# Kernel tuning notes

Hardware: AMD Instinct MI355X
Metric: run time of the kernel (lower is better)

The kernel has to match this reference:

```python
import jax, jax.numpy as jnp
import numpy as np

B, T, E, H, HD = 4, 1500, 1280, 20, 64
SCALING = HD ** -0.5


def setup_inputs() -> dict:
    key = jax.random.key(0)
    ks = jax.random.split(key, 8)
    s = 0.02
    return {
        "hidden_states": jax.random.normal(ks[0], (B, 1, T, E), jnp.float32),
        "attention_mask": jnp.zeros((B, 1, T, T), jnp.float32),
        "Wq": jax.random.normal(ks[1], (H, HD, E), jnp.float32) * s,
        "bq": jax.random.normal(ks[2], (H, HD), jnp.float32) * s,
        "Wk": jax.random.normal(ks[3], (H, HD, E), jnp.float32) * s,
        "Wv": jax.random.normal(ks[4], (H, HD, E), jnp.float32) * s,
        "bv": jax.random.normal(ks[5], (H, HD), jnp.float32) * s,
        "Wo": jax.random.normal(ks[6], (E, E), jnp.float32) * s,
        "bo": jax.random.normal(ks[7], (E,), jnp.float32) * s,
    }


def reference(hidden_states, attention_mask, Wq, bq, Wk, Wv, bv, Wo, bo):
    # hidden_states: [B, 1, T, E] (NHWC with H=1, as in the torch module)
    b, _, t, e = hidden_states.shape
    x = hidden_states[:, 0]  # [B, T, E]
    # Per-head 1x1 Conv2d projections == batched linear over stacked head weights.
    # Scaling is folded into q (the module bakes it into q_proj weights/bias).
    q = (jnp.einsum("bte,hde->bhtd", x, Wq) + bq[None, :, None, :]) * SCALING
    k = jnp.einsum("bse,hde->bhsd", x, Wk)
    v = jnp.einsum("bse,hde->bhsd", x, Wv) + bv[None, :, None, :]
    # attention_mask broadcasts over the head dim (module adds it per head as [B,1,T,S])
    scores = jnp.einsum("bhtd,bhsd->bhts", q, k) + attention_mask  # [B,H,T,S]
    attn = jax.nn.softmax(scores, axis=-1)
    out = jnp.einsum("bhts,bhsd->bhtd", attn, v)  # [B,H,T,HD]
    out = out.transpose(0, 2, 1, 3).reshape(b, t, e)  # concat heads on channel dim
    final = jnp.einsum("bte,fe->btf", out, Wo) + bo  # 1x1 Conv2d out_proj
    return final[:, None, :, :]  # [B,1,T,E]
```

## Files before the change

kernel.cpp:

```cpp
#include <hip/hip_runtime.h>

#define T_LEN 1500
#define TP    1536
#define EDIM  1280
#define NH    20
#define HD    64
#define KDIM  1280

#define LOG2E 1.4426950408889634f

#define OFF_X    ((size_t)0)
#define OFF_AO   ((size_t)0)
#define OFF_W    ((size_t)7700480)
#define OFF_WO   ((size_t)12615680)
#define OFF_Q    ((size_t)14254080)
#define OFF_K    ((size_t)22118400)
#define OFF_VT   ((size_t)29982720)

typedef float  f32x4  __attribute__((ext_vector_type(4)));
typedef float  f32x16 __attribute__((ext_vector_type(16)));
typedef short  s16x8  __attribute__((ext_vector_type(8)));
typedef __bf16 bf16x8 __attribute__((ext_vector_type(8)));
typedef unsigned short u16;
typedef unsigned int   u32;
typedef unsigned int u32x4 __attribute__((ext_vector_type(4)));

__device__ __forceinline__ f32x4 mfma_bf16(s16x8 a, s16x8 b, f32x4 c) {
  return __builtin_amdgcn_mfma_f32_16x16x32_bf16(
      __builtin_bit_cast(bf16x8, a), __builtin_bit_cast(bf16x8, b), c, 0, 0, 0);
}

__device__ __forceinline__ f32x16 mfma32(s16x8 a, s16x8 b, f32x16 c) {
  return __builtin_amdgcn_mfma_f32_32x32x16_bf16(
      __builtin_bit_cast(bf16x8, a), __builtin_bit_cast(bf16x8, b), c, 0, 0, 0);
}

__device__ __forceinline__ u16 f2bf(float f) {
  union { float f; unsigned int u; } a; a.f = f;
  return (u16)((a.u + 0x7fffu + ((a.u >> 16) & 1u)) >> 16);
}

__device__ __forceinline__ float fexp2(float x) {
  return __builtin_amdgcn_exp2f(x);
}

__device__ __forceinline__ void gl_lds16(const u16* g, u16* l) {
  __builtin_amdgcn_global_load_lds(
      (const __attribute__((address_space(1))) unsigned int*)(const void*)g,
      (__attribute__((address_space(3))) unsigned int*)(void*)l, 16, 0, 0);
}


__global__ __launch_bounds__(256) void prep_kernel(
    const float* __restrict__ x, const float* __restrict__ wq,
    const float* __restrict__ wk, const float* __restrict__ wv,
    const float* __restrict__ wo, const float* __restrict__ mask,
    u16* __restrict__ ws, u32* __restrict__ nzflags) {
  const int S0 = 1925120;
  const int S1 = 1228800;
  const int S2 = 409600;
  const int P1 = 46080;
  const int S3 = 2250000;
  const int TOT = S0 + S1 + S2 + 3 * P1 + S3;
  for (int v = blockIdx.x * 256 + threadIdx.x; v < TOT; v += gridDim.x * 256) {
    if (v < S0) {
      int i = v * 4;
      int m = i / EDIM;
      ushort4 o;
      if (m < 6000) {
        float4 f = *(const float4*)(x + i);
        o = make_ushort4(f2bf(f.x), f2bf(f.y), f2bf(f.z), f2bf(f.w));
      } else {
        o = make_ushort4(0, 0, 0, 0);
      }
      *(ushort4*)(ws + OFF_X + i) = o;
    } else if (v < S0 + S1) {
      int j = (v - S0) * 4;
      int n = j / EDIM, e = j - n * EDIM;
      const float* s = (n < 1280) ? wq + (size_t)n * EDIM + e
                     : (n < 2560) ? wk + (size_t)(n - 1280) * EDIM + e
                                  : wv + (size_t)(n - 2560) * EDIM + e;
      float4 f = *(const float4*)s;
      *(ushort4*)(ws + OFF_W + j) = make_ushort4(f2bf(f.x), f2bf(f.y), f2bf(f.z), f2bf(f.w));
    } else if (v < S0 + S1 + S2) {
      int j = (v - S0 - S1) * 4;
      float4 f = *(const float4*)(wo + j);
      *(ushort4*)(ws + OFF_WO + j) = make_ushort4(f2bf(f.x), f2bf(f.y), f2bf(f.z), f2bf(f.w));
    } else if (v < S0 + S1 + S2 + 3 * P1) {
      int p = v - (S0 + S1 + S2);
      ushort4 z = make_ushort4(0, 0, 0, 0);
      if (p < P1) {
        int p4 = p * 4; int bh = p4 / 2304; int rem = p4 - bh * 2304;
        int tt = rem >> 6, d = rem & 63;
        *(ushort4*)(ws + OFF_Q + ((size_t)(bh * TP + 1500 + tt)) * HD + d) = z;
      } else if (p < 2 * P1) {
        int p4 = (p - P1) * 4; int bh = p4 / 2304; int rem = p4 - bh * 2304;
        int tt = rem >> 6, d = rem & 63;
        *(ushort4*)(ws + OFF_K + ((size_t)(bh * TP + 1500 + tt)) * HD + d) = z;
      } else {
        int p4 = (p - 2 * P1) * 4; int bh = p4 / 2304; int rem = p4 - bh * 2304;
        int d = rem / 36, ss = rem - d * 36;
        int t = 1500 + ss;
        int tphys = (t & ~63) | (((((t >> 3) & 7) ^ (d & 7))) << 3) | (t & 7);
        *(ushort4*)(ws + OFF_VT + ((size_t)(bh * HD + d)) * TP + tphys) = z;
      }
    } else {
      int p = v - (S0 + S1 + S2 + 3 * P1);
      int i4 = p * 4;
      int bb = i4 / 2250000;
      int rem = i4 - bb * 2250000;
      int q = rem / 1500;
      int s = rem - q * 1500;
      float4 f = *(const float4*)(mask + (size_t)bb * 2250000 + rem);
      if (f.x != 0.f || f.y != 0.f || f.z != 0.f || f.w != 0.f)
        atomicOr(&nzflags[(bb * 12 + (q >> 7)) * 24 + (s >> 6)], 1u);
    }
  }
}

__device__ __forceinline__ void gemm_mainloop(
    const u16* __restrict__ A, const u16* __restrict__ B,
    int mt, int nt, u16* As, u16* Bs, f32x4 acc[4][4]) {
  const int tid = threadIdx.x;
  const int w = tid >> 6, lane = tid & 63, lg = lane >> 4, lr = lane & 15;
  const int wr = w >> 1, wc = w & 1;
  const int c0 = tid, c1 = tid + 256;
  const u16* a0 = A + (size_t)(mt * 128 + (c0 >> 2)) * KDIM + (c0 & 3) * 8;
  const u16* a1 = A + (size_t)(mt * 128 + (c1 >> 2)) * KDIM + (c1 & 3) * 8;
  const u16* b0 = B + (size_t)(nt * 128 + (c0 >> 2)) * KDIM + (c0 & 3) * 8;
  const u16* b1 = B + (size_t)(nt * 128 + (c1 >> 2)) * KDIM + (c1 & 3) * 8;
  u16* lA0 = As + c0 * 8; u16* lA1 = As + c1 * 8;
  u16* lB0 = Bs + c0 * 8; u16* lB1 = Bs + c1 * 8;
  for (int kt = 0; kt < KDIM / 32; ++kt) {
    gl_lds16(a0 + kt * 32, lA0);
    gl_lds16(a1 + kt * 32, lA1);
    gl_lds16(b0 + kt * 32, lB0);
    gl_lds16(b1 + kt * 32, lB1);
    __syncthreads();
    s16x8 af[4], bg[4];
    #pragma unroll
    for (int i = 0; i < 4; ++i) {
      af[i] = *(const s16x8*)(As + ((wr * 64 + i * 16 + lr) * 32 + lg * 8));
      bg[i] = *(const s16x8*)(Bs + ((wc * 64 + i * 16 + lr) * 32 + lg * 8));
    }
    #pragma unroll
    for (int i = 0; i < 4; ++i)
      #pragma unroll
      for (int j = 0; j < 4; ++j)
        acc[i][j] = mfma_bf16(af[i], bg[j], acc[i][j]);
    __syncthreads();
  }
}

__global__ __launch_bounds__(256) void gemm_qkv_kernel(
    const u16* __restrict__ X, const u16* __restrict__ W,
    const float* __restrict__ bq, const float* __restrict__ bv,
    u16* __restrict__ Qw, u16* __restrict__ Kw, u16* __restrict__ Vtw) {
  __shared__ __align__(16) u16 As[128 * 32];
  __shared__ __align__(16) u16 Bs[128 * 32];
  const int nt = blockIdx.x, mt = blockIdx.y;
  f32x4 acc[4][4] = {};
  gemm_mainloop(X, W, mt, nt, As, Bs, acc);
  const int tid = threadIdx.x;
  const int w = tid >> 6, lane = tid & 63, lg = lane >> 4, lr = lane & 15;
  const int wr = w >> 1, wc = w & 1;
  #pragma unroll
  for (int i = 0; i < 4; ++i) {
    #pragma unroll
    for (int r = 0; r < 4; ++r) {
      int mm = mt * 128 + wr * 64 + i * 16 + lg * 4 + r;
      if (mm >= 6000) continue;
      int bt = mm / 1500, tt = mm - bt * 1500;
      #pragma unroll
      for (int j = 0; j < 4; ++j) {
        int n = nt * 128 + wc * 64 + j * 16 + lr;
        float v = acc[i][j][r];
        if (n < 1280) {
          int hh = n >> 6, d = n & 63;
          Qw[((size_t)(bt * NH + hh) * TP + tt) * HD + d] =
              f2bf((v + bq[n]) * (0.125f * LOG2E));
        } else if (n < 2560) {
          int nn = n - 1280, hh = nn >> 6, d = nn & 63;
          int dp = ((((d >> 3) ^ (tt & 7))) << 3) | (d & 7);
          Kw[((size_t)(bt * NH + hh) * TP + tt) * HD + dp] = f2bf(v);
        } else {
          int nn = n - 2560, hh = nn >> 6, d = nn & 63;
          int tphys = (tt & ~63) | (((((tt >> 3) & 7) ^ (d & 7))) << 3) | (tt & 7);
          Vtw[((size_t)(bt * NH + hh) * HD + d) * TP + tphys] = f2bf(v + bv[nn]);
        }
      }
    }
  }
}

__global__ __launch_bounds__(256) void attn_kernel(
    const u16* __restrict__ Qw, const u16* __restrict__ Kw,
    const u16* __restrict__ Vtw, const float* __restrict__ mask,
    const u32* __restrict__ nzflags, u16* __restrict__ AO) {
  __shared__ __align__(16) u16 Kb[2][64 * 64];
  __shared__ __align__(16) u16 Vb[2][64 * 64];
  const int bhid = blockIdx.y;
  const int bb = bhid / NH, hh = bhid % NH;
  const int tid = threadIdx.x;
  const int w = tid >> 6;
  const int lane = tid & 63;
  const int lq = lane & 31;
  const int hi = lane >> 5;
  const int q0 = blockIdx.x * 128 + w * 32;
  const int qrow = q0 + lq;
  const int qm = qrow < (T_LEN - 1) ? qrow : (T_LEN - 1);
  const u16* Qp = Qw + (size_t)bhid * TP * HD;
  const u16* Kp = Kw + (size_t)bhid * TP * HD;
  const u16* Vp = Vtw + (size_t)bhid * HD * TP;
  const float* mp = mask + (size_t)bb * T_LEN * T_LEN + (size_t)qm * T_LEN;
  const u32* nzp = nzflags + (bb * 12 + blockIdx.x) * 24;

  s16x8 qf[4];
  #pragma unroll
  for (int c = 0; c < 4; ++c)
    qf[c] = *(const s16x8*)(Qp + (size_t)qrow * HD + c * 16 + hi * 8);

  f32x16 O0 = {}, O1 = {};
  float m = -3e38f, l = 0.f;

  {
    gl_lds16(Kp + tid * 8,                 Kb[0] + tid * 8);
    gl_lds16(Kp + 2048 + tid * 8,          Kb[0] + 2048 + tid * 8);
    int r = tid >> 3, g = tid & 7;
    gl_lds16(Vp + (size_t)r * TP + g * 8,          Vb[0] + tid * 8);
    gl_lds16(Vp + (size_t)(r + 32) * TP + g * 8,   Vb[0] + 2048 + tid * 8);
  }
  __syncthreads();

  int buf = 0;
  #pragma unroll 1
  for (int st = 0; st < 24; ++st) {
    const int s0 = st * 64;
    if (st < 23) {
      const int sn = s0 + 64;
      gl_lds16(Kp + (size_t)sn * HD + tid * 8,        Kb[buf ^ 1] + tid * 8);
      gl_lds16(Kp + (size_t)sn * HD + 2048 + tid * 8, Kb[buf ^ 1] + 2048 + tid * 8);
      int r = tid >> 3, g = tid & 7;
      gl_lds16(Vp + (size_t)r * TP + sn + g * 8,        Vb[buf ^ 1] + tid * 8);
      gl_lds16(Vp + (size_t)(r + 32) * TP + sn + g * 8, Vb[buf ^ 1] + 2048 + tid * 8);
    }
    const bool has_mask = nzp[st] != 0u;
    const u16* kb = Kb[buf];
    f32x16 S0a = {}, S1a = {};
    #pragma unroll
    for (int c = 0; c < 4; ++c) {
      int gc = 2 * c + hi;
      int gs = (gc ^ (lq & 7)) << 3;
      s16x8 k0 = *(const s16x8*)(kb + lq * 64 + gs);
      s16x8 k1 = *(const s16x8*)(kb + (32 + lq) * 64 + gs);
      S0a = mfma32(k0, qf[c], S0a);
      S1a = mfma32(k1, qf[c], S1a);
    }
    float p[32];
    #pragma unroll
    for (int r = 0; r < 16; ++r) { p[r] = S0a[r]; p[16 + r] = S1a[r]; }
    if (has_mask) {
      f32x4 mk[2][4];
      #pragma unroll
      for (int sh = 0; sh < 2; ++sh)
        #pragma unroll
        for (int g = 0; g < 4; ++g) {
          int sb = s0 + sh * 32 + 8 * g + 4 * hi;
          if (sb > T_LEN - 4) sb = T_LEN - 4;
          mk[sh][g] = *(const f32x4*)(mp + sb);
        }
      #pragma unroll
      for (int r = 0; r < 16; ++r) {
        p[r]      = fmaf(mk[0][r >> 2][r & 3], LOG2E, p[r]);
        p[16 + r] = fmaf(mk[1][r >> 2][r & 3], LOG2E, p[16 + r]);
      }
    }
    if (st == 23) {
      if (hi) { p[12] = p[13] = p[14] = p[15] = -1e30f; }
      #pragma unroll
      for (int r = 16; r < 32; ++r) p[r] = -1e30f;
    }
    float t1[16];
    #pragma unroll
    for (int r = 0; r < 16; ++r) t1[r] = fmaxf(p[r], p[r + 16]);
    #pragma unroll
    for (int r = 0; r < 8; ++r) t1[r] = fmaxf(t1[r], t1[r + 8]);
    float mx = fmaxf(fmaxf(fmaxf(t1[0], t1[1]), fmaxf(t1[2], t1[3])),
                     fmaxf(fmaxf(t1[4], t1[5]), fmaxf(t1[6], t1[7])));
    mx = fmaxf(mx, __shfl_xor(mx, 32));
    if (!__all(mx <= m + 8.f)) {
      float mn = fmaxf(m, mx);
      float sc = fexp2(m - mn);
      O0 *= sc; O1 *= sc; l *= sc;
      m = mn;
    }
    #pragma unroll
    for (int r = 0; r < 32; ++r) p[r] = fexp2(p[r] - m);
    float s1[16];
    #pragma unroll
    for (int r = 0; r < 16; ++r) s1[r] = p[r] + p[r + 16];
    #pragma unroll
    for (int r = 0; r < 8; ++r) s1[r] += s1[r + 8];
    #pragma unroll
    for (int r = 0; r < 4; ++r) s1[r] += s1[r + 4];
    float rs = (s1[0] + s1[1]) + (s1[2] + s1[3]);
    rs += __shfl_xor(rs, 32);
    l += rs;
    const u16* vb = Vb[buf];
    #pragma unroll
    for (int sh = 0; sh < 2; ++sh) {
      u32 pk[8];
      #pragma unroll
      for (int j = 0; j < 8; ++j)
        asm("v_cvt_pk_bf16_f32 %0, %1, %2"
            : "=v"(pk[j]) : "v"(p[sh * 16 + 2 * j]), "v"(p[sh * 16 + 2 * j + 1]));
      asm("v_permlane32_swap_b32 %0, %1" : "+v"(pk[0]), "+v"(pk[2]));
      asm("v_permlane32_swap_b32 %0, %1" : "+v"(pk[1]), "+v"(pk[3]));
      asm("v_permlane32_swap_b32 %0, %1" : "+v"(pk[4]), "+v"(pk[6]));
      asm("v_permlane32_swap_b32 %0, %1" : "+v"(pk[5]), "+v"(pk[7]));
      u32x4 ta = {pk[0], pk[1], pk[2], pk[3]};
      u32x4 tb = {pk[4], pk[5], pk[6], pk[7]};
      s16x8 pfa = __builtin_bit_cast(s16x8, ta);
      s16x8 pfb = __builtin_bit_cast(s16x8, tb);
      int ga = sh * 4 + hi, gb = sh * 4 + 2 + hi;
      {
        int d = lq;
        s16x8 va = *(const s16x8*)(vb + d * 64 + ((ga ^ (d & 7)) << 3));
        s16x8 vc = *(const s16x8*)(vb + d * 64 + ((gb ^ (d & 7)) << 3));
        O0 = mfma32(va, pfa, O0);
        O0 = mfma32(vc, pfb, O0);
      }
      {
        int d = 32 + lq;
        s16x8 va = *(const s16x8*)(vb + d * 64 + ((ga ^ (d & 7)) << 3));
        s16x8 vc = *(const s16x8*)(vb + d * 64 + ((gb ^ (d & 7)) << 3));
        O1 = mfma32(va, pfa, O1);
        O1 = mfma32(vc, pfb, O1);
      }
    }
    __syncthreads();
    buf ^= 1;
  }

  if (qrow < T_LEN) {
    float inv = 1.f / l;
    size_t base = ((size_t)(bb * T_LEN + qrow)) * EDIM + hh * HD;
    #pragma unroll
    for (int g = 0; g < 4; ++g) {
      ushort4 o0, o1;
      o0.x = f2bf(O0[4 * g + 0] * inv); o0.y = f2bf(O0[4 * g + 1] * inv);
      o0.z = f2bf(O0[4 * g + 2] * inv); o0.w = f2bf(O0[4 * g + 3] * inv);
      o1.x = f2bf(O1[4 * g + 0] * inv); o1.y = f2bf(O1[4 * g + 1] * inv);
      o1.z = f2bf(O1[4 * g + 2] * inv); o1.w = f2bf(O1[4 * g + 3] * inv);
      *(ushort4*)(AO + base + 8 * g + 4 * hi)      = o0;
      *(ushort4*)(AO + base + 32 + 8 * g + 4 * hi) = o1;
    }
  }
}

__global__ __launch_bounds__(256) void gemm_out_kernel(
    const u16* __restrict__ AOb, const u16* __restrict__ Wob,
    const float* __restrict__ bo, float* __restrict__ out) {
  __shared__ __align__(16) u16 As[128 * 32];
  __shared__ __align__(16) u16 Bs[128 * 32];
  const int nt = blockIdx.x, mt = blockIdx.y;
  f32x4 acc[4][4] = {};
  gemm_mainloop(AOb, Wob, mt, nt, As, Bs, acc);
  const int tid = threadIdx.x;
  const int w = tid >> 6, lane = tid & 63, lg = lane >> 4, lr = lane & 15;
  const int wr = w >> 1, wc = w & 1;
  #pragma unroll
  for (int i = 0; i < 4; ++i) {
    #pragma unroll
    for (int r = 0; r < 4; ++r) {
      int mm = mt * 128 + wr * 64 + i * 16 + lg * 4 + r;
      if (mm >= 6000) continue;
      #pragma unroll
      for (int j = 0; j < 4; ++j) {
        int n = nt * 128 + wc * 64 + j * 16 + lr;
        out[(size_t)mm * EDIM + n] = acc[i][j][r] + bo[n];
      }
    }
  }
}

extern "C" void kernel_launch(void* const* d_in, const int* in_sizes, int n_in,
                              void* d_out, int out_size, void* d_ws, size_t ws_size,
                              hipStream_t stream) {
  const float* x    = (const float*)d_in[0];
  const float* mask = (const float*)d_in[1];
  const float* wq   = (const float*)d_in[2];
  const float* bq   = (const float*)d_in[3];
  const float* wk   = (const float*)d_in[4];
  const float* wv   = (const float*)d_in[5];
  const float* bv   = (const float*)d_in[6];
  const float* wo   = (const float*)d_in[7];
  const float* bo   = (const float*)d_in[8];
  float* out = (float*)d_out;
  u16* ws = (u16*)d_ws;
  u32* nzflags = (u32*)d_out;

  hipMemsetAsync(nzflags, 0, 1152 * sizeof(u32), stream);
  prep_kernel<<<2048, 256, 0, stream>>>(x, wq, wk, wv, wo, mask, ws, nzflags);
  gemm_qkv_kernel<<<dim3(30, 47), 256, 0, stream>>>(
      ws + OFF_X, ws + OFF_W, bq, bv, ws + OFF_Q, ws + OFF_K, ws + OFF_VT);
  attn_kernel<<<dim3(12, 80), 256, 0, stream>>>(
      ws + OFF_Q, ws + OFF_K, ws + OFF_VT, mask, nzflags, ws + OFF_AO);
  gemm_out_kernel<<<dim3(10, 47), 256, 0, stream>>>(
      ws + OFF_AO, ws + OFF_WO, bo, out);
}
```

Before: 262.7 us.

## Triple-buffer GEMM LDS loads with async prefetch and XCD-aware tile mapping

Reworks the shared GEMM mainloop to triple-buffer the LDS tiles. Global-to-LDS loads for step k+2 are issued while step k computes, and explicit vmcnt waits plus a single barrier replace the two __syncthreads per iteration. Both GEMM kernels now run on a 1D grid whose block IDs are remapped so that each XCD takes a contiguous band of M-tiles, aiming for better L2 reuse. This adds 48 M-tiles instead of 47, so some blocks do redundant loads whose stores are all masked off, and it triples the LDS footprint per block.

```diff
diff --git a/kernel.cpp b/kernel.cpp
--- a/kernel.cpp
+++ b/kernel.cpp
@@ -129,26 +129,37 @@
   const u16* a1 = A + (size_t)(mt * 128 + (c1 >> 2)) * KDIM + (c1 & 3) * 8;
   const u16* b0 = B + (size_t)(nt * 128 + (c0 >> 2)) * KDIM + (c0 & 3) * 8;
   const u16* b1 = B + (size_t)(nt * 128 + (c1 >> 2)) * KDIM + (c1 & 3) * 8;
-  u16* lA0 = As + c0 * 8; u16* lA1 = As + c1 * 8;
-  u16* lB0 = Bs + c0 * 8; u16* lB1 = Bs + c1 * 8;
-  for (int kt = 0; kt < KDIM / 32; ++kt) {
-    gl_lds16(a0 + kt * 32, lA0);
-    gl_lds16(a1 + kt * 32, lA1);
-    gl_lds16(b0 + kt * 32, lB0);
-    gl_lds16(b1 + kt * 32, lB1);
-    __syncthreads();
+  const int l0 = c0 * 8, l1 = c1 * 8;
+  const int ra = wr * 64, rb = wc * 64;
+  gl_lds16(a0,      As + l0);        gl_lds16(a1,      As + l1);
+  gl_lds16(b0,      Bs + l0);        gl_lds16(b1,      Bs + l1);
+  gl_lds16(a0 + 32, As + 4096 + l0); gl_lds16(a1 + 32, As + 4096 + l1);
+  gl_lds16(b0 + 32, Bs + 4096 + l0); gl_lds16(b1 + 32, Bs + 4096 + l1);
+  int oc = 0, on1 = 4096, on2 = 8192;
+  #pragma unroll 1
+  for (int kt = 0; kt < 40; ++kt) {
+    if (kt < 39) asm volatile("s_waitcnt vmcnt(4)" ::: "memory");
+    else         asm volatile("s_waitcnt vmcnt(0)" ::: "memory");
+    __builtin_amdgcn_s_barrier();
+    __builtin_amdgcn_sched_barrier(0);
+    if (kt < 38) {
+      gl_lds16(a0 + (kt + 2) * 32, As + on2 + l0);
+      gl_lds16(a1 + (kt + 2) * 32, As + on2 + l1);
+      gl_lds16(b0 + (kt + 2) * 32, Bs + on2 + l0);
+      gl_lds16(b1 + (kt + 2) * 32, Bs + on2 + l1);
+    }
     s16x8 af[4], bg[4];
     #pragma unroll
     for (int i = 0; i < 4; ++i) {
-      af[i] = *(const s16x8*)(As + ((wr * 64 + i * 16 + lr) * 32 + lg * 8));
-      bg[i] = *(const s16x8*)(Bs + ((wc * 64 + i * 16 + lr) * 32 + lg * 8));
+      af[i] = *(const s16x8*)(As + oc + (ra + i * 16 + lr) * 32 + lg * 8);
+      bg[i] = *(const s16x8*)(Bs + oc + (rb + i * 16 + lr) * 32 + lg * 8);
     }
     #pragma unroll
     for (int i = 0; i < 4; ++i)
       #pragma unroll
       for (int j = 0; j < 4; ++j)
         acc[i][j] = mfma_bf16(af[i], bg[j], acc[i][j]);
-    __syncthreads();
+    int t = oc; oc = on1; on1 = on2; on2 = t;
   }
 }
 
@@ -156,9 +167,12 @@
     const u16* __restrict__ X, const u16* __restrict__ W,
     const float* __restrict__ bq, const float* __restrict__ bv,
     u16* __restrict__ Qw, u16* __restrict__ Kw, u16* __restrict__ Vtw) {
-  __shared__ __align__(16) u16 As[128 * 32];
-  __shared__ __align__(16) u16 Bs[128 * 32];
-  const int nt = blockIdx.x, mt = blockIdx.y;
+  __shared__ __align__(16) u16 As[3 * 4096];
+  __shared__ __align__(16) u16 Bs[3 * 4096];
+  const int bid = blockIdx.x;
+  const int xcd = bid & 7, idx = bid >> 3;
+  const int mt = xcd * 6 + idx % 6;
+  const int nt = idx / 6;
   f32x4 acc[4][4] = {};
   gemm_mainloop(X, W, mt, nt, As, Bs, acc);
   const int tid = threadIdx.x;
@@ -361,9 +375,12 @@
 __global__ __launch_bounds__(256) void gemm_out_kernel(
     const u16* __restrict__ AOb, const u16* __restrict__ Wob,
     const float* __restrict__ bo, float* __restrict__ out) {
-  __shared__ __align__(16) u16 As[128 * 32];
-  __shared__ __align__(16) u16 Bs[128 * 32];
-  const int nt = blockIdx.x, mt = blockIdx.y;
+  __shared__ __align__(16) u16 As[3 * 4096];
+  __shared__ __align__(16) u16 Bs[3 * 4096];
+  const int bid = blockIdx.x;
+  const int xcd = bid & 7, idx = bid >> 3;
+  const int mt = xcd * 6 + idx % 6;
+  const int nt = idx / 6;
   f32x4 acc[4][4] = {};
   gemm_mainloop(AOb, Wob, mt, nt, As, Bs, acc);
   const int tid = threadIdx.x;
@@ -402,10 +419,10 @@
 
   hipMemsetAsync(nzflags, 0, 1152 * sizeof(u32), stream);
   prep_kernel<<<2048, 256, 0, stream>>>(x, wq, wk, wv, wo, mask, ws, nzflags);
-  gemm_qkv_kernel<<<dim3(30, 47), 256, 0, stream>>>(
+  gemm_qkv_kernel<<<1440, 256, 0, stream>>>(
       ws + OFF_X, ws + OFF_W, bq, bv, ws + OFF_Q, ws + OFF_K, ws + OFF_VT);
   attn_kernel<<<dim3(12, 80), 256, 0, stream>>>(
       ws + OFF_Q, ws + OFF_K, ws + OFF_VT, mask, nzflags, ws + OFF_AO);
-  gemm_out_kernel<<<dim3(10, 47), 256, 0, stream>>>(
+  gemm_out_kernel<<<480, 256, 0, stream>>>(
       ws + OFF_AO, ws + OFF_WO, bo, out);
 }
```

New measurement: 252.6 us. 3.9% less time.

## Rewrite GEMMs with 256x128 tiles, triple-buffered LDS prefetch, swizzled layout

Applied to the files above, without the earlier changes.

Replaces the single-buffered 128x128 GEMM mainloop with a 512-thread, 256x128-tile loop. It uses a three-stage LDS ring, keeps global-to-LDS loads for k-step kt+2 in flight while computing kt, and raises wave priority around the MFMA blocks. Operands are written pre-swizzled (XOR on 8-element groups) in the prep and attention epilogues so LDS reads avoid bank conflicts. Block indices are remapped so M tiles are grouped per XCD for L2 reuse. The aim is to hide global load latency and cut LDS conflicts and barrier stalls, at the cost of larger LDS use (about 144KB per block) and lower occupancy.

```diff
diff --git a/kernel.cpp b/kernel.cpp
--- a/kernel.cpp
+++ b/kernel.cpp
@@ -6,6 +6,7 @@
 #define NH    20
 #define HD    64
 #define KDIM  1280
+#define NT    20
 
 #define LOG2E 1.4426950408889634f
 
@@ -65,7 +66,8 @@
   for (int v = blockIdx.x * 256 + threadIdx.x; v < TOT; v += gridDim.x * 256) {
     if (v < S0) {
       int i = v * 4;
-      int m = i / EDIM;
+      int m = i / EDIM, e = i - m * EDIM;
+      int ep = (e & ~63) | (((((e >> 3) & 7) ^ (m & 7))) << 3) | (e & 7);
       ushort4 o;
       if (m < 6000) {
         float4 f = *(const float4*)(x + i);
@@ -73,7 +75,7 @@
       } else {
         o = make_ushort4(0, 0, 0, 0);
       }
-      *(ushort4*)(ws + OFF_X + i) = o;
+      *(ushort4*)(ws + OFF_X + (size_t)m * EDIM + ep) = o;
     } else if (v < S0 + S1) {
       int j = (v - S0) * 4;
       int n = j / EDIM, e = j - n * EDIM;
@@ -81,11 +83,16 @@
                      : (n < 2560) ? wk + (size_t)(n - 1280) * EDIM + e
                                   : wv + (size_t)(n - 2560) * EDIM + e;
       float4 f = *(const float4*)s;
-      *(ushort4*)(ws + OFF_W + j) = make_ushort4(f2bf(f.x), f2bf(f.y), f2bf(f.z), f2bf(f.w));
+      int ep = (e & ~63) | (((((e >> 3) & 7) ^ (n & 7))) << 3) | (e & 7);
+      *(ushort4*)(ws + OFF_W + (size_t)n * EDIM + ep) =
+          make_ushort4(f2bf(f.x), f2bf(f.y), f2bf(f.z), f2bf(f.w));
     } else if (v < S0 + S1 + S2) {
       int j = (v - S0 - S1) * 4;
+      int n = j / EDIM, e = j - n * EDIM;
       float4 f = *(const float4*)(wo + j);
-      *(ushort4*)(ws + OFF_WO + j) = make_ushort4(f2bf(f.x), f2bf(f.y), f2bf(f.z), f2bf(f.w));
+      int ep = (e & ~63) | (((((e >> 3) & 7) ^ (n & 7))) << 3) | (e & 7);
+      *(ushort4*)(ws + OFF_WO + (size_t)n * EDIM + ep) =
+          make_ushort4(f2bf(f.x), f2bf(f.y), f2bf(f.z), f2bf(f.w));
     } else if (v < S0 + S1 + S2 + 3 * P1) {
       int p = v - (S0 + S1 + S2);
       ushort4 z = make_ushort4(0, 0, 0, 0);
@@ -118,62 +125,127 @@
   }
 }
 
-__device__ __forceinline__ void gemm_mainloop(
+__device__ __forceinline__ void gemm_mainloop256(
     const u16* __restrict__ A, const u16* __restrict__ B,
-    int mt, int nt, u16* As, u16* Bs, f32x4 acc[4][4]) {
+    int mt, int nt, u16* lds, f32x4 acc[4][4]) {
   const int tid = threadIdx.x;
-  const int w = tid >> 6, lane = tid & 63, lg = lane >> 4, lr = lane & 15;
-  const int wr = w >> 1, wc = w & 1;
-  const int c0 = tid, c1 = tid + 256;
-  const u16* a0 = A + (size_t)(mt * 128 + (c0 >> 2)) * KDIM + (c0 & 3) * 8;
-  const u16* a1 = A + (size_t)(mt * 128 + (c1 >> 2)) * KDIM + (c1 & 3) * 8;
-  const u16* b0 = B + (size_t)(nt * 128 + (c0 >> 2)) * KDIM + (c0 & 3) * 8;
-  const u16* b1 = B + (size_t)(nt * 128 + (c1 >> 2)) * KDIM + (c1 & 3) * 8;
-  u16* lA0 = As + c0 * 8; u16* lA1 = As + c1 * 8;
-  u16* lB0 = Bs + c0 * 8; u16* lB1 = Bs + c1 * 8;
-  for (int kt = 0; kt < KDIM / 32; ++kt) {
-    gl_lds16(a0 + kt * 32, lA0);
-    gl_lds16(a1 + kt * 32, lA1);
-    gl_lds16(b0 + kt * 32, lB0);
-    gl_lds16(b1 + kt * 32, lB1);
-    __syncthreads();
-    s16x8 af[4], bg[4];
-    #pragma unroll
-    for (int i = 0; i < 4; ++i) {
-      af[i] = *(const s16x8*)(As + ((wr * 64 + i * 16 + lr) * 32 + lg * 8));
-      bg[i] = *(const s16x8*)(Bs + ((wc * 64 + i * 16 + lr) * 32 + lg * 8));
-    }
-    #pragma unroll
-    for (int i = 0; i < 4; ++i)
-      #pragma unroll
-      for (int j = 0; j < 4; ++j)
-        acc[i][j] = mfma_bf16(af[i], bg[j], acc[i][j]);
-    __syncthreads();
-  }
-}
-
-__global__ __launch_bounds__(256) void gemm_qkv_kernel(
+  const int lane = tid & 63, wid = tid >> 6;
+  const int lg = lane >> 4, lr = lane & 15;
+  const int wr = wid >> 1, wn = wid & 1;
+
+  const u16* aB = A + (size_t)(mt * 256) * KDIM;
+  const u16* bB = B + (size_t)(nt * 128) * KDIM;
+  size_t aOff[4], bOff[2];
+  #pragma unroll
+  for (int l = 0; l < 4; ++l) {
+    int gid = l * 512 + tid;
+    aOff[l] = (size_t)(gid >> 3) * KDIM + (gid & 7) * 8;
+  }
+  #pragma unroll
+  for (int l = 0; l < 2; ++l) {
+    int gid = l * 512 + tid;
+    bOff[l] = (size_t)(gid >> 3) * KDIM + (gid & 7) * 8;
+  }
+  const int ldsOff = tid * 8;
+  int arow[4], brow[4];
+  #pragma unroll
+  for (int i = 0; i < 4; ++i) arow[i] = (wr * 64 + i * 16 + lr) * 64;
+  #pragma unroll
+  for (int j = 0; j < 4; ++j) brow[j] = (wn * 64 + j * 16 + lr) * 64;
+  const int gsw0 = ((lg) ^ (lr & 7)) * 8;
+  const int gsw1 = ((4 + lg) ^ (lr & 7)) * 8;
+
+  #pragma unroll
+  for (int t = 0; t < 2; ++t) {
+    u16* dA = lds + t * 24576;
+    u16* dB = dA + 16384;
+    #pragma unroll
+    for (int l = 0; l < 4; ++l) gl_lds16(aB + aOff[l] + t * 64, dA + ldsOff + l * 4096);
+    #pragma unroll
+    for (int l = 0; l < 2; ++l) gl_lds16(bB + bOff[l] + t * 64, dB + ldsOff + l * 4096);
+  }
+
+  int s = 0;
+  #pragma unroll 1
+  for (int kt = 0; kt < NT; ++kt) {
+    if (kt < NT - 1) asm volatile("s_waitcnt vmcnt(6)" ::: "memory");
+    else             asm volatile("s_waitcnt vmcnt(0)" ::: "memory");
+    __builtin_amdgcn_s_barrier();
+    __builtin_amdgcn_sched_barrier(0);
+    u16* cA = lds + s * 24576;
+    u16* cB = cA + 16384;
+    int ssl = s + 2; if (ssl >= 3) ssl -= 3;
+    u16* sA = lds + ssl * 24576;
+    u16* sB = sA + 16384;
+    const bool doStage = (kt + 2 < NT);
+    if (doStage) {
+      gl_lds16(aB + aOff[0] + (kt + 2) * 64, sA + ldsOff);
+      gl_lds16(aB + aOff[1] + (kt + 2) * 64, sA + ldsOff + 4096);
+      gl_lds16(bB + bOff[0] + (kt + 2) * 64, sB + ldsOff);
+    }
+    {
+      s16x8 af[4], bg[4];
+      #pragma unroll
+      for (int i = 0; i < 4; ++i) af[i] = *(const s16x8*)(cA + arow[i] + gsw0);
+      #pragma unroll
+      for (int j = 0; j < 4; ++j) bg[j] = *(const s16x8*)(cB + brow[j] + gsw0);
+      __builtin_amdgcn_s_setprio(1);
+      #pragma unroll
+      for (int i = 0; i < 4; ++i)
+        #pragma unroll
+        for (int j = 0; j < 4; ++j)
+          acc[i][j] = mfma_bf16(af[i], bg[j], acc[i][j]);
+      __builtin_amdgcn_s_setprio(0);
+    }
+    __builtin_amdgcn_s_barrier();
+    if (doStage) {
+      gl_lds16(aB + aOff[2] + (kt + 2) * 64, sA + ldsOff + 8192);
+      gl_lds16(aB + aOff[3] + (kt + 2) * 64, sA + ldsOff + 12288);
+      gl_lds16(bB + bOff[1] + (kt + 2) * 64, sB + ldsOff + 4096);
+    }
+    {
+      s16x8 af[4], bg[4];
+      #pragma unroll
+      for (int i = 0; i < 4; ++i) af[i] = *(const s16x8*)(cA + arow[i] + gsw1);
+      #pragma unroll
+      for (int j = 0; j < 4; ++j) bg[j] = *(const s16x8*)(cB + brow[j] + gsw1);
+      __builtin_amdgcn_s_setprio(1);
+      #pragma unroll
+      for (int i = 0; i < 4; ++i)
+        #pragma unroll
+        for (int j = 0; j < 4; ++j)
+          acc[i][j] = mfma_bf16(af[i], bg[j], acc[i][j]);
+      __builtin_amdgcn_s_setprio(0);
+    }
+    s = s + 1; if (s >= 3) s = 0;
+  }
+}
+
+__global__ __launch_bounds__(512) void gemm_qkv_kernel(
     const u16* __restrict__ X, const u16* __restrict__ W,
     const float* __restrict__ bq, const float* __restrict__ bv,
     u16* __restrict__ Qw, u16* __restrict__ Kw, u16* __restrict__ Vtw) {
-  __shared__ __align__(16) u16 As[128 * 32];
-  __shared__ __align__(16) u16 Bs[128 * 32];
-  const int nt = blockIdx.x, mt = blockIdx.y;
+  __shared__ __align__(16) u16 lds[3 * 24576];
+  const int bid = blockIdx.x;
+  const int xcd = bid & 7, idx = bid >> 3;
+  const int mt = xcd * 3 + idx % 3;
+  const int nt = idx / 3;
   f32x4 acc[4][4] = {};
-  gemm_mainloop(X, W, mt, nt, As, Bs, acc);
+  gemm_mainloop256(X, W, mt, nt, lds, acc);
   const int tid = threadIdx.x;
-  const int w = tid >> 6, lane = tid & 63, lg = lane >> 4, lr = lane & 15;
-  const int wr = w >> 1, wc = w & 1;
+  const int lane = tid & 63, wid = tid >> 6;
+  const int lg = lane >> 4, lr = lane & 15;
+  const int wr = wid >> 1, wn = wid & 1;
   #pragma unroll
   for (int i = 0; i < 4; ++i) {
     #pragma unroll
     for (int r = 0; r < 4; ++r) {
-      int mm = mt * 128 + wr * 64 + i * 16 + lg * 4 + r;
+      int mm = mt * 256 + wr * 64 + i * 16 + lg * 4 + r;
       if (mm >= 6000) continue;
       int bt = mm / 1500, tt = mm - bt * 1500;
       #pragma unroll
       for (int j = 0; j < 4; ++j) {
-        int n = nt * 128 + wc * 64 + j * 16 + lr;
+        int n = nt * 128 + wn * 64 + j * 16 + lr;
         float v = acc[i][j][r];
         if (n < 1280) {
           int hh = n >> 6, d = n & 63;
@@ -344,7 +416,9 @@
 
   if (qrow < T_LEN) {
     float inv = 1.f / l;
-    size_t base = ((size_t)(bb * T_LEN + qrow)) * EDIM + hh * HD;
+    int arow = bb * T_LEN + qrow;
+    int key = arow & 7;
+    size_t base = (size_t)arow * EDIM + hh * 64;
     #pragma unroll
     for (int g = 0; g < 4; ++g) {
       ushort4 o0, o1;
@@ -352,32 +426,35 @@
       o0.z = f2bf(O0[4 * g + 2] * inv); o0.w = f2bf(O0[4 * g + 3] * inv);
       o1.x = f2bf(O1[4 * g + 0] * inv); o1.y = f2bf(O1[4 * g + 1] * inv);
       o1.z = f2bf(O1[4 * g + 2] * inv); o1.w = f2bf(O1[4 * g + 3] * inv);
-      *(ushort4*)(AO + base + 8 * g + 4 * hi)      = o0;
-      *(ushort4*)(AO + base + 32 + 8 * g + 4 * hi) = o1;
-    }
-  }
-}
-
-__global__ __launch_bounds__(256) void gemm_out_kernel(
+      *(ushort4*)(AO + base + ((g ^ key) << 3) + 4 * hi)       = o0;
+      *(ushort4*)(AO + base + (((4 + g) ^ key) << 3) + 4 * hi) = o1;
+    }
+  }
+}
+
+__global__ __launch_bounds__(512) void gemm_out_kernel(
     const u16* __restrict__ AOb, const u16* __restrict__ Wob,
     const float* __restrict__ bo, float* __restrict__ out) {
-  __shared__ __align__(16) u16 As[128 * 32];
-  __shared__ __align__(16) u16 Bs[128 * 32];
-  const int nt = blockIdx.x, mt = blockIdx.y;
+  __shared__ __align__(16) u16 lds[3 * 24576];
+  const int bid = blockIdx.x;
+  const int xcd = bid & 7, idx = bid >> 3;
+  const int mt = xcd * 3 + idx % 3;
+  const int nt = idx / 3;
   f32x4 acc[4][4] = {};
-  gemm_mainloop(AOb, Wob, mt, nt, As, Bs, acc);
+  gemm_mainloop256(AOb, Wob, mt, nt, lds, acc);
   const int tid = threadIdx.x;
-  const int w = tid >> 6, lane = tid & 63, lg = lane >> 4, lr = lane & 15;
-  const int wr = w >> 1, wc = w & 1;
+  const int lane = tid & 63, wid = tid >> 6;
+  const int lg = lane >> 4, lr = lane & 15;
+  const int wr = wid >> 1, wn = wid & 1;
   #pragma unroll
   for (int i = 0; i < 4; ++i) {
     #pragma unroll
     for (int r = 0; r < 4; ++r) {
-      int mm = mt * 128 + wr * 64 + i * 16 + lg * 4 + r;
+      int mm = mt * 256 + wr * 64 + i * 16 + lg * 4 + r;
       if (mm >= 6000) continue;
       #pragma unroll
       for (int j = 0; j < 4; ++j) {
-        int n = nt * 128 + wc * 64 + j * 16 + lr;
+        int n = nt * 128 + wn * 64 + j * 16 + lr;
         out[(size_t)mm * EDIM + n] = acc[i][j][r] + bo[n];
       }
     }
@@ -402,10 +479,10 @@
 
   hipMemsetAsync(nzflags, 0, 1152 * sizeof(u32), stream);
   prep_kernel<<<2048, 256, 0, stream>>>(x, wq, wk, wv, wo, mask, ws, nzflags);
-  gemm_qkv_kernel<<<dim3(30, 47), 256, 0, stream>>>(
+  gemm_qkv_kernel<<<720, 512, 0, stream>>>(
       ws + OFF_X, ws + OFF_W, bq, bv, ws + OFF_Q, ws + OFF_K, ws + OFF_VT);
   attn_kernel<<<dim3(12, 80), 256, 0, stream>>>(
       ws + OFF_Q, ws + OFF_K, ws + OFF_VT, mask, nzflags, ws + OFF_AO);
-  gemm_out_kernel<<<dim3(10, 47), 256, 0, stream>>>(
+  gemm_out_kernel<<<240, 512, 0, stream>>>(
       ws + OFF_AO, ws + OFF_WO, bo, out);
 }
```

Result: faster. 244.4 us (-7.0%).
